# Kernel tuning notes

Measured on AMD Instinct MI355X. Metric: run time of the kernel, lower is better.

Reference implementation:

```python
import jax, jax.numpy as jnp
import numpy as np

N, D = 131072, 512

def setup_inputs() -> dict:
    key = jax.random.key(0)
    k1, k2, k3 = jax.random.split(key, 3)
    feature = jax.random.normal(k1, (N, D), dtype=jnp.float32)
    mean = jax.random.normal(k2, (D,), dtype=jnp.float32)
    inverse_cov = jax.random.normal(k3, (D, D), dtype=jnp.float32)
    return {"feature": feature, "mean": mean, "inverse_cov": inverse_cov}

def reference(feature, mean, inverse_cov):
    # zero_f: [N, D]
    zero_f = feature - mean
    # diag(zero_f @ inv_cov @ zero_f.T) == rowwise quadratic form,
    # computed without the NxN intermediate: (zero_f @ inv_cov * zero_f).sum(-1)
    quad = jnp.einsum('nd,de,ne->n', zero_f, inverse_cov, zero_f)
    return jnp.mean(quad)
```

## Files before the change

kernel.cpp:

```cpp
#include <hip/hip_runtime.h>
#include <hip/hip_bf16.h>
#include <stdint.h>


typedef __attribute__((ext_vector_type(8))) short short8;
typedef __attribute__((ext_vector_type(4))) float floatx4;

static constexpr int NROWS = 131072;
static constexpr int DDIM  = 512;
static constexpr int BM = 128, BN = 128, BK = 32;
static constexpr int FS_STRIDE = 136;
static constexpr int BS_STRIDE = 40;

__device__ __forceinline__ short f2bf(float f) {
  __bf16 b = (__bf16)f;
  return __builtin_bit_cast(short, b);
}
__device__ __forceinline__ float bf2f(short s) {
  __bf16 b = __builtin_bit_cast(__bf16, s);
  return (float)b;
}

__global__ __launch_bounds__(256) void maha_prep(const float* __restrict__ C,
                                                 const float* __restrict__ mean,
                                                 short* __restrict__ Ct,
                                                 float* __restrict__ w,
                                                 float* __restrict__ out) {
  const int e = blockIdx.x;
  const int t = threadIdx.x;
  float c0 = C[t * DDIM + e];
  float c1 = C[(t + 256) * DDIM + e];
  short b0 = f2bf(c0), b1 = f2bf(c1);
  Ct[e * DDIM + t]       = b0;
  Ct[e * DDIM + t + 256] = b1;
  float p = mean[t] * bf2f(b0) + mean[t + 256] * bf2f(b1);
  __shared__ float red[256];
  red[t] = p;
  __syncthreads();
  for (int off = 128; off > 0; off >>= 1) {
    if (t < off) red[t] += red[t + off];
    __syncthreads();
  }
  if (t == 0) {
    w[e] = red[0];
    if (e == 0) out[0] = 0.0f;
  }
}

__global__ __launch_bounds__(256, 3) void maha_main(const float* __restrict__ F,
                                                    const float* __restrict__ mean,
                                                    const short* __restrict__ Ct,
                                                    const float* __restrict__ w,
                                                    float* __restrict__ out) {
  __shared__ short Fs[BM * FS_STRIDE];
  __shared__ short Bs[BN * BS_STRIDE];
  __shared__ float red[4];

  const int b = blockIdx.x;
  const int mtile = ((b >> 5) << 3) | (b & 7);
  const int etile = (b >> 3) & 3;
  const int m0 = mtile * BM;
  const int e0 = etile * BN;

  const int t    = threadIdx.x;
  const int lane = t & 63;
  const int wave = t >> 6;
  const int wm = wave >> 1, wn = wave & 1;
  const int l15  = lane & 15;
  const int quad = lane >> 4;

  const int rA = t >> 1;
  const int hA = t & 1;
  const float* Fbase = F  + (size_t)(m0 + rA) * DDIM + hA * 16;
  const short* Cbase = Ct + (size_t)(e0 + rA) * DDIM + hA * 16;

  floatx4 pa[4];
  short8  pb0, pb1;
  const int chunk_base = (e0 >> 5) + 4;

  auto loadpf = [&](int c) {
    const int ch = (chunk_base + c) & 15;
    const floatx4* fp = (const floatx4*)(Fbase + ch * 32);
    pa[0] = fp[0]; pa[1] = fp[1]; pa[2] = fp[2]; pa[3] = fp[3];
    const short8* bp = (const short8*)(Cbase + ch * 32);
    pb0 = bp[0]; pb1 = bp[1];
  };

  floatx4 acc[4][4];
#pragma unroll
  for (int i = 0; i < 4; i++)
#pragma unroll
    for (int j = 0; j < 4; j++) acc[i][j] = floatx4{0.f, 0.f, 0.f, 0.f};

  loadpf(0);

#pragma unroll 4
  for (int c = 0; c < 16; ++c) {
    const int s = c & 3;
    __syncthreads();
    short8 w0, w1;
#pragma unroll
    for (int q = 0; q < 2; q++)
#pragma unroll
      for (int k = 0; k < 4; k++) {
        w0[q * 4 + k] = f2bf(pa[q][k]);
        w1[q * 4 + k] = f2bf(pa[q + 2][k]);
      }
    *(short8*)&Fs[rA * FS_STRIDE + s * 32 + hA * 16]     = w0;
    *(short8*)&Fs[rA * FS_STRIDE + s * 32 + hA * 16 + 8] = w1;
    *(short8*)&Bs[rA * BS_STRIDE + hA * 16]              = pb0;
    *(short8*)&Bs[rA * BS_STRIDE + hA * 16 + 8]          = pb1;
    if (c < 15) loadpf(c + 1);
    __syncthreads();

    short8 af[4], bfv[4];
#pragma unroll
    for (int i = 0; i < 4; i++)
      af[i] = *(const short8*)&Fs[(wm * 64 + i * 16 + l15) * FS_STRIDE + s * 32 + quad * 8];
#pragma unroll
    for (int j = 0; j < 4; j++)
      bfv[j] = *(const short8*)&Bs[(wn * 64 + j * 16 + l15) * BS_STRIDE + quad * 8];
#pragma unroll
    for (int i = 0; i < 4; i++)
#pragma unroll
      for (int j = 0; j < 4; j++)
        acc[i][j] = __builtin_amdgcn_mfma_f32_16x16x32_bf16(af[i], bfv[j], acc[i][j], 0, 0, 0);
  }

  float psum = 0.f;
#pragma unroll
  for (int j = 0; j < 4; j++) {
    const int e_loc = wn * 64 + j * 16 + l15;
    const float wj = w[e0 + e_loc];
    const float mj = mean[e0 + e_loc];
#pragma unroll
    for (int i = 0; i < 4; i++) {
      const int m_base = wm * 64 + i * 16 + quad * 4;
#pragma unroll
      for (int r = 0; r < 4; r++) {
        const float fv = bf2f(Fs[(m_base + r) * FS_STRIDE + e_loc]);
        psum += (acc[i][j][r] - wj) * (fv - mj);
      }
    }
  }

#pragma unroll
  for (int off = 32; off > 0; off >>= 1) psum += __shfl_down(psum, off);
  if (lane == 0) red[wave] = psum;
  __syncthreads();
  if (t == 0) {
    const float tot = (red[0] + red[1] + red[2] + red[3]) * (1.0f / (float)NROWS);
    atomicAdd(out, tot);
  }
}

extern "C" void kernel_launch(void* const* d_in, const int* in_sizes, int n_in,
                              void* d_out, int out_size, void* d_ws, size_t ws_size,
                              hipStream_t stream) {
  const float* feature = (const float*)d_in[0];
  const float* mean    = (const float*)d_in[1];
  const float* invcov  = (const float*)d_in[2];
  float* out = (float*)d_out;

  float* w  = (float*)d_ws;
  short* Ct = (short*)((char*)d_ws + 4096);

  maha_prep<<<512, 256, 0, stream>>>(invcov, mean, Ct, w, out);
  maha_main<<<4096, 256, 0, stream>>>(feature, mean, Ct, w, out);
}
```

Before: 429.9 us.

## Deepen main-loop global prefetch to two stages and tile the inverse-covariance transpose

The main GEMM loop now keeps two register stages of prefetched feature and Ct data, issuing loads two chunks ahead and fully unrolling the loop, so global memory latency is better hidden. The prep kernel is split into a shared-memory tiled transpose with coalesced reads and writes, plus a single-block kernel that computes the mean-weighted column sums. The extra prefetch stage raises register pressure, which may reduce occupancy under the 3-blocks-per-SM launch bound. The single-block w kernel is serial and may cost more than it saves.

```diff
diff --git a/kernel.cpp b/kernel.cpp
--- a/kernel.cpp
+++ b/kernel.cpp
@@ -8,7 +8,7 @@
 
 static constexpr int NROWS = 131072;
 static constexpr int DDIM  = 512;
-static constexpr int BM = 128, BN = 128, BK = 32;
+static constexpr int BM = 128, BN = 128;
 static constexpr int FS_STRIDE = 136;
 static constexpr int BS_STRIDE = 40;
 
@@ -21,30 +21,45 @@
   return (float)b;
 }
 
-__global__ __launch_bounds__(256) void maha_prep(const float* __restrict__ C,
-                                                 const float* __restrict__ mean,
-                                                 short* __restrict__ Ct,
-                                                 float* __restrict__ w,
-                                                 float* __restrict__ out) {
-  const int e = blockIdx.x;
-  const int t = threadIdx.x;
-  float c0 = C[t * DDIM + e];
-  float c1 = C[(t + 256) * DDIM + e];
-  short b0 = f2bf(c0), b1 = f2bf(c1);
-  Ct[e * DDIM + t]       = b0;
-  Ct[e * DDIM + t + 256] = b1;
-  float p = mean[t] * bf2f(b0) + mean[t + 256] * bf2f(b1);
-  __shared__ float red[256];
-  red[t] = p;
+__global__ __launch_bounds__(256) void maha_prep_t(const float* __restrict__ C,
+                                                   short* __restrict__ Ct) {
+  __shared__ short T[128 * FS_STRIDE];
+  const int bt = blockIdx.x;
+  const int k0 = (bt & 3) * 128;
+  const int e0 = (bt >> 2) * 128;
+  const int rr = threadIdx.x >> 5;
+  const int cc = threadIdx.x & 31;
+#pragma unroll
+  for (int p = 0; p < 16; p++) {
+    const int k = p * 8 + rr;
+    floatx4 v = *(const floatx4*)(C + (size_t)(k0 + k) * DDIM + e0 + cc * 4);
+#pragma unroll
+    for (int i = 0; i < 4; i++) T[(cc * 4 + i) * FS_STRIDE + k] = f2bf(v[i]);
+  }
   __syncthreads();
-  for (int off = 128; off > 0; off >>= 1) {
-    if (t < off) red[t] += red[t + off];
-    __syncthreads();
+  const int er = threadIdx.x >> 4;
+  const int kc = threadIdx.x & 15;
+#pragma unroll
+  for (int p = 0; p < 8; p++) {
+    const int e = p * 16 + er;
+    short8 v = *(const short8*)&T[e * FS_STRIDE + kc * 8];
+    *(short8*)(Ct + (size_t)(e0 + e) * DDIM + k0 + kc * 8) = v;
   }
-  if (t == 0) {
-    w[e] = red[0];
-    if (e == 0) out[0] = 0.0f;
+}
+
+__global__ __launch_bounds__(512) void maha_prep_w(const float* __restrict__ C,
+                                                   const float* __restrict__ mean,
+                                                   float* __restrict__ w,
+                                                   float* __restrict__ out) {
+  const int e = threadIdx.x;
+  float acc = 0.f;
+  for (int k = 0; k < DDIM; k += 8) {
+#pragma unroll
+    for (int i = 0; i < 8; i++)
+      acc += mean[k + i] * bf2f(f2bf(C[(size_t)(k + i) * DDIM + e]));
   }
+  w[e] = acc;
+  if (e == 0) out[0] = 0.0f;
 }
 
 __global__ __launch_bounds__(256, 3) void maha_main(const float* __restrict__ F,
@@ -74,16 +89,16 @@
   const float* Fbase = F  + (size_t)(m0 + rA) * DDIM + hA * 16;
   const short* Cbase = Ct + (size_t)(e0 + rA) * DDIM + hA * 16;
 
-  floatx4 pa[4];
-  short8  pb0, pb1;
+  floatx4 pa[2][4];
+  short8  pb[2][2];
   const int chunk_base = (e0 >> 5) + 4;
 
-  auto loadpf = [&](int c) {
+  auto loadpf = [&](int c, int st) {
     const int ch = (chunk_base + c) & 15;
     const floatx4* fp = (const floatx4*)(Fbase + ch * 32);
-    pa[0] = fp[0]; pa[1] = fp[1]; pa[2] = fp[2]; pa[3] = fp[3];
+    pa[st][0] = fp[0]; pa[st][1] = fp[1]; pa[st][2] = fp[2]; pa[st][3] = fp[3];
     const short8* bp = (const short8*)(Cbase + ch * 32);
-    pb0 = bp[0]; pb1 = bp[1];
+    pb[st][0] = bp[0]; pb[st][1] = bp[1];
   };
 
   floatx4 acc[4][4];
@@ -92,25 +107,27 @@
 #pragma unroll
     for (int j = 0; j < 4; j++) acc[i][j] = floatx4{0.f, 0.f, 0.f, 0.f};
 
-  loadpf(0);
+  loadpf(0, 0);
+  loadpf(1, 1);
 
-#pragma unroll 4
+#pragma unroll
   for (int c = 0; c < 16; ++c) {
-    const int s = c & 3;
+    const int s  = c & 3;
+    const int st = c & 1;
     __syncthreads();
     short8 w0, w1;
 #pragma unroll
     for (int q = 0; q < 2; q++)
 #pragma unroll
       for (int k = 0; k < 4; k++) {
-        w0[q * 4 + k] = f2bf(pa[q][k]);
-        w1[q * 4 + k] = f2bf(pa[q + 2][k]);
+        w0[q * 4 + k] = f2bf(pa[st][q][k]);
+        w1[q * 4 + k] = f2bf(pa[st][q + 2][k]);
       }
     *(short8*)&Fs[rA * FS_STRIDE + s * 32 + hA * 16]     = w0;
     *(short8*)&Fs[rA * FS_STRIDE + s * 32 + hA * 16 + 8] = w1;
-    *(short8*)&Bs[rA * BS_STRIDE + hA * 16]              = pb0;
-    *(short8*)&Bs[rA * BS_STRIDE + hA * 16 + 8]          = pb1;
-    if (c < 15) loadpf(c + 1);
+    *(short8*)&Bs[rA * BS_STRIDE + hA * 16]              = pb[st][0];
+    *(short8*)&Bs[rA * BS_STRIDE + hA * 16 + 8]          = pb[st][1];
+    if (c < 14) loadpf(c + 2, st);
     __syncthreads();
 
     short8 af[4], bfv[4];
@@ -165,6 +182,7 @@
   float* w  = (float*)d_ws;
   short* Ct = (short*)((char*)d_ws + 4096);
 
-  maha_prep<<<512, 256, 0, stream>>>(invcov, mean, Ct, w, out);
+  maha_prep_t<<<16, 256, 0, stream>>>(invcov, Ct);
+  maha_prep_w<<<1, 512, 0, stream>>>(invcov, mean, w, out);
   maha_main<<<4096, 256, 0, stream>>>(feature, mean, Ct, w, out);
 }
```

Result: slower. 461.7 us (+7.4%).
